# Performance work log

Measured on AMD Instinct MI355X. Metric: run time of the kernel, lower is better.

The kernel has to match this reference:

```python
import jax, jax.numpy as jnp
import numpy as np

N_CUST, N_PROD, N_EDGES, EMBED_DIM, HIDDEN = 100000, 100000, 1000000, 64, 64


def setup_inputs() -> dict:
    key = jax.random.key(0)
    ks = jax.random.split(key, 8)
    D = EMBED_DIM
    return {
        "h_customer": jax.random.normal(ks[0], (N_CUST, D), dtype=jnp.float32),
        "h_product": jax.random.normal(ks[1], (N_PROD, D), dtype=jnp.float32),
        "src_idx": jax.random.randint(ks[2], (N_EDGES,), 0, N_CUST),
        "dst_idx": jax.random.randint(ks[3], (N_EDGES,), 0, N_PROD),
        "W1": jax.random.normal(ks[4], (2 * D + 1, HIDDEN), dtype=jnp.float32) * 0.05,
        "b1": jnp.zeros((HIDDEN,), dtype=jnp.float32),
        "W2": jax.random.normal(ks[5], (HIDDEN, 1), dtype=jnp.float32) * 0.05,
        "b2": jnp.zeros((1,), dtype=jnp.float32),
    }


def reference(h_customer, h_product, src_idx, dst_idx, W1, b1, W2, b2):
    # Per-edge gather of head/tail node embeddings: [E, D]
    heads = h_customer[src_idx]
    tails = h_product[dst_idx]

    # F.normalize(p=2, dim=-1), torch eps = 1e-12
    hn = heads / jnp.maximum(jnp.linalg.norm(heads, axis=-1, keepdims=True), 1e-12)
    tn = tails / jnp.maximum(jnp.linalg.norm(tails, axis=-1, keepdims=True), 1e-12)

    # cosine_similarity of already-normalized vectors, torch eps = 1e-8
    denom = jnp.maximum(
        jnp.linalg.norm(hn, axis=-1) * jnp.linalg.norm(tn, axis=-1), 1e-8
    )
    cos = jnp.sum(hn * tn, axis=-1) / denom  # [E]

    # concat(raw heads, raw tails, cosine) -> [E, 2D+1]
    cat = jnp.concatenate([heads, tails, cos[:, None]], axis=1)

    # small prediction MLP -> sigmoid ratings, [E, 1]
    x = jax.nn.relu(cat @ W1 + b1)
    ratings = jax.nn.sigmoid(x @ W2 + b2)
    return ratings
```

## Files before the change

### kernel.cpp

```cpp
#include <hip/hip_runtime.h>
#include <math.h>


typedef __attribute__((ext_vector_type(8))) short bf16x8;
typedef __attribute__((ext_vector_type(4))) float f32x4;
typedef __attribute__((ext_vector_type(2))) float float2_t;
typedef __attribute__((ext_vector_type(8))) unsigned short ushort8_t;
typedef __attribute__((ext_vector_type(4))) float float4_t;
typedef __attribute__((ext_vector_type(4))) unsigned int uint4_t;
typedef __attribute__((ext_vector_type(2))) unsigned int uint2_t;

#define P_STRIDE 72

__device__ __forceinline__ float bf2f(unsigned short u) {
    return __uint_as_float(((unsigned int)u) << 16);
}
__device__ __forceinline__ unsigned short f2bf(float f) {
    unsigned int x = __float_as_uint(f);
    return (unsigned short)((x + 0x7fffu + ((x >> 16) & 1u)) >> 16);
}

__global__ __launch_bounds__(256) void prep_w1(
    const float* __restrict__ W1, unsigned short* __restrict__ frag)
{
    int idx = blockIdx.x * 256 + threadIdx.x;
    if (idx >= 2 * 4 * 2 * 64 * 8) return;
    int j    = idx & 7;
    int lane = (idx >> 3) & 63;
    int ks   = (idx >> 9) & 1;
    int nt   = (idx >> 10) & 3;
    int half = (idx >> 12) & 1;
    int k   = ks * 32 + (lane >> 4) * 8 + j;
    int col = nt * 16 + (lane & 15);
    frag[idx] = f2bf(W1[(half * 64 + k) * 64 + col]);
}

__global__ __launch_bounds__(256) void node_fused(
    const float* __restrict__ hc, const float* __restrict__ hp,
    const unsigned short* __restrict__ w1frag, const float* __restrict__ b1,
    unsigned char* __restrict__ recC, unsigned char* __restrict__ recP,
    int nC, int nP, int blocksC)
{
    __shared__ unsigned short tile2[64 * P_STRIDE];

    int b = blockIdx.x;
    const float* h; unsigned char* rec; int n, half;
    if (b < blocksC) { h = hc; rec = recC; n = nC; half = 0; }
    else { b -= blocksC; h = hp; rec = recP; n = nP; half = 1; }

    int node0 = b * 64;
    int nloc  = min(64, n - node0);
    int t     = threadIdx.x;
    int wave  = t >> 6, lane = t & 63;
    int m = lane & 15, quad = lane >> 4;

    if (wave * 16 < nloc) {
        int row = node0 + wave * 16 + m;
        float4_t f[2][2];
#pragma unroll
        for (int ks = 0; ks < 2; ks++) {
            const float* srcp = h + (long)row * 64 + ks * 32 + quad * 8;
            f[ks][0] = *reinterpret_cast<const float4_t*>(srcp);
            f[ks][1] = *reinterpret_cast<const float4_t*>(srcp + 4);
        }

        float ss = 0.f;
#pragma unroll
        for (int ks = 0; ks < 2; ks++)
#pragma unroll
            for (int i = 0; i < 2; i++)
#pragma unroll
                for (int j = 0; j < 4; j++) ss += f[ks][i][j] * f[ks][i][j];
        ss += __shfl_xor(ss, 16);
        ss += __shfl_xor(ss, 32);
        float inv = 1.f / fmaxf(sqrtf(ss), 1e-12f);

#pragma unroll
        for (int ks = 0; ks < 2; ks++) {
            uint2_t u8;
#pragma unroll
            for (int i = 0; i < 2; i++) {
                unsigned int d = __builtin_amdgcn_cvt_pk_fp8_f32(
                    f[ks][i][0] * inv, f[ks][i][1] * inv, 0, false);
                d = __builtin_amdgcn_cvt_pk_fp8_f32(
                    f[ks][i][2] * inv, f[ks][i][3] * inv, d, true);
                u8[i] = d;
            }
            *reinterpret_cast<uint2_t*>(rec + (long)row * 128 + ks * 32 + quad * 8) = u8;
        }

        bf16x8 a[2];
#pragma unroll
        for (int ks = 0; ks < 2; ks++)
#pragma unroll
            for (int i = 0; i < 8; i++)
                a[ks][i] = (short)f2bf(f[ks][i >> 2][i & 3]);

        f32x4 acc[4];
#pragma unroll
        for (int nt = 0; nt < 4; nt++) acc[nt] = (f32x4){0.f, 0.f, 0.f, 0.f};
#pragma unroll
        for (int nt = 0; nt < 4; nt++)
#pragma unroll
            for (int ks = 0; ks < 2; ks++) {
                bf16x8 bf = *reinterpret_cast<const bf16x8*>(
                    &w1frag[(((half * 4 + nt) * 2 + ks) * 64 + lane) * 8]);
                acc[nt] = __builtin_amdgcn_mfma_f32_16x16x32_bf16(
                    a[ks], bf, acc[nt], 0, 0, 0);
            }
        if (half == 0) {
#pragma unroll
            for (int nt = 0; nt < 4; nt++) {
                float bb = b1[nt * 16 + m];
#pragma unroll
                for (int r = 0; r < 4; r++) acc[nt][r] += bb;
            }
        }
#pragma unroll
        for (int nt = 0; nt < 4; nt++)
#pragma unroll
            for (int r = 0; r < 4; r++)
                tile2[(wave * 16 + quad * 4 + r) * P_STRIDE + nt * 16 + m]
                    = f2bf(acc[nt][r]);
    }
    __syncthreads();

    int nl = t >> 2, q = t & 3;
    if (nl < nloc) {
        ushort8_t p0 = *reinterpret_cast<ushort8_t*>(&tile2[nl * P_STRIDE + q * 16]);
        ushort8_t p1 = *reinterpret_cast<ushort8_t*>(&tile2[nl * P_STRIDE + q * 16 + 8]);
        float v[16];
#pragma unroll
        for (int i = 0; i < 8; i++) { v[i] = bf2f(p0[i]); v[i + 8] = bf2f(p1[i]); }
        uint4_t u;
#pragma unroll
        for (int i = 0; i < 4; i++) {
            unsigned int d = __builtin_amdgcn_cvt_pk_fp8_f32(
                v[i * 4 + 0], v[i * 4 + 1], 0, false);
            d = __builtin_amdgcn_cvt_pk_fp8_f32(
                v[i * 4 + 2], v[i * 4 + 3], d, true);
            u[i] = d;
        }
        *reinterpret_cast<uint4_t*>(rec + (long)(node0 + nl) * 128 + 64 + q * 16) = u;
    }
}

__global__ __launch_bounds__(256) void edge_mlp(
    const unsigned char* __restrict__ recC, const unsigned char* __restrict__ recP,
    const int* __restrict__ src, const int* __restrict__ dst,
    const float* __restrict__ W1, const float* __restrict__ W2,
    const float* __restrict__ b2, float* __restrict__ out, int nE)
{
    int lane = threadIdx.x & 63;
    int sub  = lane >> 2;
    int g    = lane & 3;
    int d0   = g * 16;
    int e    = ((blockIdx.x * 256 + threadIdx.x) >> 6) * 16 + sub;
    bool valid = e < nE;
    int s = valid ? src[e] : 0;
    int t = valid ? dst[e] : 0;

    const unsigned char* rs = recC + (long)s * 128;
    const unsigned char* rt = recP + (long)t * 128;
    uint4_t hs = *reinterpret_cast<const uint4_t*>(rs + d0);
    uint4_t ht = *reinterpret_cast<const uint4_t*>(rt + d0);
    uint4_t ps = *reinterpret_cast<const uint4_t*>(rs + 64 + d0);
    uint4_t pt = *reinterpret_cast<const uint4_t*>(rt + 64 + d0);

    float4_t w1v[4], w2v[4];
#pragma unroll
    for (int i = 0; i < 4; i++) {
        w1v[i] = *reinterpret_cast<const float4_t*>(W1 + 128 * 64 + d0 + i * 4);
        w2v[i] = *reinterpret_cast<const float4_t*>(W2 + d0 + i * 4);
    }
    float b2v = b2[0];

    float dot = 0.f;
#pragma unroll
    for (int w = 0; w < 4; w++) {
        float2_t alo = __builtin_amdgcn_cvt_pk_f32_fp8((int)hs[w], false);
        float2_t ahi = __builtin_amdgcn_cvt_pk_f32_fp8((int)hs[w], true);
        float2_t blo = __builtin_amdgcn_cvt_pk_f32_fp8((int)ht[w], false);
        float2_t bhi = __builtin_amdgcn_cvt_pk_f32_fp8((int)ht[w], true);
        dot += alo[0] * blo[0] + alo[1] * blo[1] + ahi[0] * bhi[0] + ahi[1] * bhi[1];
    }
    dot += __shfl_xor(dot, 1);
    dot += __shfl_xor(dot, 2);
    float cosv = dot;

    float p = 0.f;
#pragma unroll
    for (int w = 0; w < 4; w++) {
        float2_t clo = __builtin_amdgcn_cvt_pk_f32_fp8((int)ps[w], false);
        float2_t chi = __builtin_amdgcn_cvt_pk_f32_fp8((int)ps[w], true);
        float2_t dlo = __builtin_amdgcn_cvt_pk_f32_fp8((int)pt[w], false);
        float2_t dhi = __builtin_amdgcn_cvt_pk_f32_fp8((int)pt[w], true);
        float pcv[4] = {clo[0], clo[1], chi[0], chi[1]};
        float ppv[4] = {dlo[0], dlo[1], dhi[0], dhi[1]};
#pragma unroll
        for (int j = 0; j < 4; j++) {
            float x = pcv[j] + ppv[j] + cosv * w1v[w][j];
            x = fmaxf(x, 0.f);
            p += x * w2v[w][j];
        }
    }
    p += __shfl_xor(p, 1);
    p += __shfl_xor(p, 2);

    if (valid && g == 0)
        out[e] = 1.f / (1.f + expf(-(p + b2v)));
}

extern "C" void kernel_launch(void* const* d_in, const int* in_sizes, int n_in,
                              void* d_out, int out_size, void* d_ws, size_t ws_size,
                              hipStream_t stream) {
    const float* h_c = (const float*)d_in[0];
    const float* h_p = (const float*)d_in[1];
    const int*   src = (const int*)d_in[2];
    const int*   dst = (const int*)d_in[3];
    const float* W1  = (const float*)d_in[4];
    const float* b1  = (const float*)d_in[5];
    const float* W2  = (const float*)d_in[6];
    const float* b2  = (const float*)d_in[7];
    float* out = (float*)d_out;

    int nC = in_sizes[0] / 64;
    int nP = in_sizes[1] / 64;
    int nE = in_sizes[2];

    char* ws = (char*)d_ws;
    size_t off = 0;
    auto carve = [&](size_t bytes) {
        void* p = ws + off;
        off = (off + bytes + 255) & ~(size_t)255;
        return p;
    };
    unsigned char* recC = (unsigned char*)carve((size_t)nC * 128);
    unsigned char* recP = (unsigned char*)carve((size_t)nP * 128);
    unsigned short* w1f = (unsigned short*)carve((size_t)16384 * 2);

    prep_w1<<<64, 256, 0, stream>>>(W1, w1f);

    int blocksC = (nC + 63) / 64, blocksP = (nP + 63) / 64;
    node_fused<<<blocksC + blocksP, 256, 0, stream>>>(
        h_c, h_p, w1f, b1, recC, recP, nC, nP, blocksC);

    edge_mlp<<<(nE + 63) / 64, 256, 0, stream>>>(
        recC, recP, src, dst, W1, W2, b2, out, nE);
}
```

Measured before the change: 148.3 us.

## Stage node loads and record writes through LDS for coalesced global access

The node kernel now reads each node row contiguously, with four threads per node, computes the norm with a shuffle, and writes the bf16 copy into an LDS tile. The MFMA A fragments are then read from that tile instead of strided global loads. Both the fp8 normalized half and the projected half of each record are assembled in an LDS buffer and written out with contiguous 32-byte-per-thread stores. This aims to coalesce global reads and writes, at the cost of more LDS, two more barriers and lower occupancy.

```diff
diff --git a/kernel.cpp b/kernel.cpp
--- a/kernel.cpp
+++ b/kernel.cpp
@@ -10,6 +10,7 @@
 typedef __attribute__((ext_vector_type(4))) unsigned int uint4_t;
 typedef __attribute__((ext_vector_type(2))) unsigned int uint2_t;
 
+#define T_STRIDE 72
 #define P_STRIDE 72
 
 __device__ __forceinline__ float bf2f(unsigned short u) {
@@ -41,7 +42,9 @@
     unsigned char* __restrict__ recC, unsigned char* __restrict__ recP,
     int nC, int nP, int blocksC)
 {
+    __shared__ unsigned short tileA[64 * T_STRIDE];
     __shared__ unsigned short tile2[64 * P_STRIDE];
+    __shared__ unsigned char  recs[64 * 128];
 
     int b = blockIdx.x;
     const float* h; unsigned char* rec; int n, half;
@@ -51,50 +54,51 @@
     int node0 = b * 64;
     int nloc  = min(64, n - node0);
     int t     = threadIdx.x;
+    int nl    = t >> 2, q = t & 3;
     int wave  = t >> 6, lane = t & 63;
     int m = lane & 15, quad = lane >> 4;
 
+    if (nl < nloc) {
+        const float* srcp = h + (long)(node0 + nl) * 64 + q * 16;
+        float4_t v[4];
+#pragma unroll
+        for (int i = 0; i < 4; i++)
+            v[i] = *reinterpret_cast<const float4_t*>(srcp + i * 4);
+
+        float ss = 0.f;
+#pragma unroll
+        for (int i = 0; i < 4; i++)
+#pragma unroll
+            for (int j = 0; j < 4; j++) ss += v[i][j] * v[i][j];
+        ss += __shfl_xor(ss, 1);
+        ss += __shfl_xor(ss, 2);
+        float inv = 1.f / fmaxf(sqrtf(ss), 1e-12f);
+
+        ushort8_t u[2];
+#pragma unroll
+        for (int i = 0; i < 16; i++) u[i >> 3][i & 7] = f2bf(v[i >> 2][i & 3]);
+        *reinterpret_cast<ushort8_t*>(&tileA[nl * T_STRIDE + q * 16])     = u[0];
+        *reinterpret_cast<ushort8_t*>(&tileA[nl * T_STRIDE + q * 16 + 8]) = u[1];
+
+        uint4_t u8;
+#pragma unroll
+        for (int i = 0; i < 4; i++) {
+            unsigned int d = __builtin_amdgcn_cvt_pk_fp8_f32(
+                v[i][0] * inv, v[i][1] * inv, 0, false);
+            d = __builtin_amdgcn_cvt_pk_fp8_f32(
+                v[i][2] * inv, v[i][3] * inv, d, true);
+            u8[i] = d;
+        }
+        *reinterpret_cast<uint4_t*>(&recs[nl * 128 + q * 16]) = u8;
+    }
+    __syncthreads();
+
     if (wave * 16 < nloc) {
-        int row = node0 + wave * 16 + m;
-        float4_t f[2][2];
-#pragma unroll
-        for (int ks = 0; ks < 2; ks++) {
-            const float* srcp = h + (long)row * 64 + ks * 32 + quad * 8;
-            f[ks][0] = *reinterpret_cast<const float4_t*>(srcp);
-            f[ks][1] = *reinterpret_cast<const float4_t*>(srcp + 4);
-        }
-
-        float ss = 0.f;
+        bf16x8 a[2];
 #pragma unroll
         for (int ks = 0; ks < 2; ks++)
-#pragma unroll
-            for (int i = 0; i < 2; i++)
-#pragma unroll
-                for (int j = 0; j < 4; j++) ss += f[ks][i][j] * f[ks][i][j];
-        ss += __shfl_xor(ss, 16);
-        ss += __shfl_xor(ss, 32);
-        float inv = 1.f / fmaxf(sqrtf(ss), 1e-12f);
-
-#pragma unroll
-        for (int ks = 0; ks < 2; ks++) {
-            uint2_t u8;
-#pragma unroll
-            for (int i = 0; i < 2; i++) {
-                unsigned int d = __builtin_amdgcn_cvt_pk_fp8_f32(
-                    f[ks][i][0] * inv, f[ks][i][1] * inv, 0, false);
-                d = __builtin_amdgcn_cvt_pk_fp8_f32(
-                    f[ks][i][2] * inv, f[ks][i][3] * inv, d, true);
-                u8[i] = d;
-            }
-            *reinterpret_cast<uint2_t*>(rec + (long)row * 128 + ks * 32 + quad * 8) = u8;
-        }
-
-        bf16x8 a[2];
-#pragma unroll
-        for (int ks = 0; ks < 2; ks++)
-#pragma unroll
-            for (int i = 0; i < 8; i++)
-                a[ks][i] = (short)f2bf(f[ks][i >> 2][i & 3]);
+            a[ks] = *reinterpret_cast<const bf16x8*>(
+                &tileA[(wave * 16 + m) * T_STRIDE + ks * 32 + quad * 8]);
 
         f32x4 acc[4];
 #pragma unroll
@@ -125,7 +129,6 @@
     }
     __syncthreads();
 
-    int nl = t >> 2, q = t & 3;
     if (nl < nloc) {
         ushort8_t p0 = *reinterpret_cast<ushort8_t*>(&tile2[nl * P_STRIDE + q * 16]);
         ushort8_t p1 = *reinterpret_cast<ushort8_t*>(&tile2[nl * P_STRIDE + q * 16 + 8]);
@@ -141,7 +144,16 @@
                 v[i * 4 + 2], v[i * 4 + 3], d, true);
             u[i] = d;
         }
-        *reinterpret_cast<uint4_t*>(rec + (long)(node0 + nl) * 128 + 64 + q * 16) = u;
+        *reinterpret_cast<uint4_t*>(&recs[nl * 128 + 64 + q * 16]) = u;
+    }
+    __syncthreads();
+
+    if (t * 32 < nloc * 128) {
+        uint4_t r0 = *reinterpret_cast<uint4_t*>(&recs[t * 32]);
+        uint4_t r1 = *reinterpret_cast<uint4_t*>(&recs[t * 32 + 16]);
+        unsigned char* dstp = rec + (long)node0 * 128 + t * 32;
+        *reinterpret_cast<uint4_t*>(dstp)      = r0;
+        *reinterpret_cast<uint4_t*>(dstp + 16) = r1;
     }
 }
 
```

Measured after the change: 148.2 us. No clear change (-0.1%).
